# Optimization experiments

Hardware: AMD Instinct MI355X
Metric: run time of the kernel (lower is better)

## Reference

```python
import jax, jax.numpy as jnp
import numpy as np


def setup_inputs() -> dict:
    key = jax.random.key(0)
    ks = jax.random.split(key, 5)
    B, C, D, H, W = 2, 256, 8, 28, 28
    mid = C // 2
    # Kaiming-normal-ish init (std = sqrt(2/fan_in)) for 1x1 conv weights
    def kaiming(k, shape, fan_in):
        return jax.random.normal(k, shape, dtype=jnp.float32) * np.sqrt(2.0 / fan_in)
    x = jax.random.normal(ks[0], (B, C, D, H, W), dtype=jnp.float32)
    w1 = kaiming(ks[1], (mid, C), C)
    w2 = kaiming(ks[2], (mid, C), C)
    w3 = kaiming(ks[3], (mid, C), C)
    w4 = kaiming(ks[4], (C, mid), mid)
    b1 = jnp.zeros((mid,), jnp.float32)
    b2 = jnp.zeros((mid,), jnp.float32)
    b3 = jnp.zeros((mid,), jnp.float32)
    b4 = jnp.zeros((C,), jnp.float32)
    return {"x": x, "w1": w1, "b1": b1, "w2": w2, "b2": b2,
            "w3": w3, "b3": b3, "w4": w4, "b4": b4}


def reference(x, w1, b1, w2, b2, w3, b3, w4, b4):
    # x: [B, C, D, H, W]; 1x1x1 Conv3d == channel matmul over flattened N = D*H*W
    B, C, D, H, W = x.shape
    N = D * H * W
    xf = x.reshape(B, C, N)                                   # [B, C, N]
    # theta: conv1 -> [B, N, mid]
    e1 = jnp.einsum('mc,bcn->bnm', w1, xf) + b1               # [B, N, mid]
    # phi: conv2 -> [B, mid, N]
    e2 = jnp.einsum('mc,bcn->bmn', w2, xf) + b2[:, None]      # [B, mid, N]
    # g: conv3 -> [B, N, mid]
    e3 = jnp.einsum('mc,bcn->bnm', w3, xf) + b3               # [B, N, mid]
    # unscaled attention: softmax over keys (last axis)
    kernel = jnp.einsum('bnm,bmk->bnk', e1, e2)               # [B, N, N]
    kernel = jax.nn.softmax(kernel, axis=2)
    attn = jnp.einsum('bnk,bkm->bnm', kernel, e3)             # [B, N, mid]
    # conv4 (1x1 Conv1d): mid -> C, applied on [B, mid, N]
    y = jnp.einsum('cm,bnm->bcn', w4, attn) + b4[:, None]     # [B, C, N]
    return x + y.reshape(B, C, D, H, W)
```

## Files before the change

### kernel.cpp

```cpp
#include <hip/hip_runtime.h>


#define BB  2
#define CC  256
#define NN  6272
#define MID 128
#define KS  4
#define QB  128
#define NT  (NN / 64)
#define LOG2E 1.4426950408889634f

typedef _Float16 half2_t __attribute__((ext_vector_type(2)));
typedef _Float16 half4_t __attribute__((ext_vector_type(4)));
typedef _Float16 half8_t __attribute__((ext_vector_type(8)));
typedef float    floatx16 __attribute__((ext_vector_type(16)));
typedef int      i32x2 __attribute__((ext_vector_type(2)));
typedef unsigned u32x4 __attribute__((ext_vector_type(4)));

__device__ __forceinline__ void fma4(float4& a, const float4 v, const float s) {
    a.x += v.x * s; a.y += v.y * s; a.z += v.z * s; a.w += v.w * s;
}
__device__ __forceinline__ float dot4(const float4 a, const float4 b) {
    return a.x * b.x + a.y * b.y + a.z * b.z + a.w * b.w;
}
__device__ __forceinline__ unsigned pkrtz(float a, float b) {
    return __builtin_bit_cast(unsigned, __builtin_amdgcn_cvt_pkrtz(a, b));
}

__global__ __launch_bounds__(256, 2) void proj_kernel(
    const float* __restrict__ x,
    const float* __restrict__ w1, const float* __restrict__ bi1,
    const float* __restrict__ w2, const float* __restrict__ bi2,
    const float* __restrict__ w3, const float* __restrict__ bi3,
    _Float16* __restrict__ Qg, _Float16* __restrict__ Kg, _Float16* __restrict__ VtG)
{
    const int t  = threadIdx.x;
    const int n0 = blockIdx.x * 64;
    const int pj = blockIdx.y;
    const int b  = blockIdx.z;
    const float* w  = (pj == 0) ? w1 : (pj == 1) ? w2 : w3;
    const float* bi = (pj == 0) ? bi1 : (pj == 1) ? bi2 : bi3;
    const float qs  = (pj == 0) ? LOG2E : 1.0f;

    __shared__ float xs[CC * 68];
    {
        const float* xb = x + (size_t)b * CC * NN;
        for (int r = t; r < CC * 16; r += 256) {
            int c = r >> 4, j = (r & 15) << 2;
            float4 v = *(const float4*)(xb + (size_t)c * NN + n0 + j);
            *(float4*)&xs[c * 68 + j] = v;
        }
    }
    __syncthreads();

    const int n4 = (t & 15) << 2;
    const int m0 = (t >> 4) << 3;
    float4 acc4[8];
    #pragma unroll
    for (int k = 0; k < 8; ++k) acc4[k] = make_float4(0.f, 0.f, 0.f, 0.f);

    for (int cc = 0; cc < CC; cc += 4) {
        float4 xv[4];
        #pragma unroll
        for (int u = 0; u < 4; ++u)
            xv[u] = *(const float4*)&xs[(cc + u) * 68 + n4];
        #pragma unroll
        for (int k = 0; k < 8; ++k) {
            float4 wq = *(const float4*)(w + (size_t)(m0 + k) * CC + cc);
            fma4(acc4[k], xv[0], wq.x);
            fma4(acc4[k], xv[1], wq.y);
            fma4(acc4[k], xv[2], wq.z);
            fma4(acc4[k], xv[3], wq.w);
        }
    }

    const float* af = (const float*)acc4;
    float bb[8];
    #pragma unroll
    for (int k = 0; k < 8; ++k) bb[k] = bi[m0 + k];

    if (pj < 2) {
        _Float16* eo = ((pj == 0) ? Qg : Kg) + (size_t)b * NN * MID;
        #pragma unroll
        for (int i = 0; i < 4; ++i) {
            half8_t h;
            #pragma unroll
            for (int k = 0; k < 8; ++k) h[k] = (_Float16)((af[k * 4 + i] + bb[k]) * qs);
            *(half8_t*)(eo + (size_t)(n0 + n4 + i) * MID + m0) = h;
        }
    } else {
        _Float16* eo = VtG + (size_t)b * MID * NN;
        #pragma unroll
        for (int k = 0; k < 8; ++k) {
            half4_t h;
            #pragma unroll
            for (int i = 0; i < 4; ++i) h[i] = (_Float16)(af[k * 4 + i] + bb[k]);
            *(half4_t*)(eo + (size_t)(m0 + k) * NN + n0 + n4) = h;
        }
    }
}

__global__ __launch_bounds__(256, 2) void attn_kernel(
    const _Float16* __restrict__ Qg, const _Float16* __restrict__ Kg,
    const _Float16* __restrict__ VtG, _Float16* __restrict__ Opart,
    float* __restrict__ MLg)
{
    const int t    = threadIdx.x;
    const int lane = t & 63;
    const int wave = t >> 6;
    const int l31  = lane & 31;
    const int l5   = lane >> 5;
    const int q0   = blockIdx.x * QB;
    const int sp   = blockIdx.y;
    const int b    = blockIdx.z;
    const int kt0  = (NT * sp) / KS;
    const int kt1  = (NT * (sp + 1)) / KS;

    __shared__ __align__(16) char lds[34816];
    _Float16* Ks  = (_Float16*)lds;
    _Float16* Vt  = (_Float16*)(lds + 17408);
    _Float16* Osh = (_Float16*)lds;

    const _Float16* Qb = Qg + ((size_t)b * NN + q0 + wave * 32) * MID;
    const _Float16* Kb = Kg + (size_t)b * NN * MID;
    const _Float16* Vb = VtG + (size_t)b * MID * NN;

    half8_t qf[8];
    #pragma unroll
    for (int ds = 0; ds < 8; ++ds)
        qf[ds] = *(const half8_t*)(Qb + (size_t)l31 * MID + ds * 16 + l5 * 8);

    floatx16 o[4];
    #pragma unroll
    for (int dt = 0; dt < 4; ++dt)
        #pragma unroll
        for (int j = 0; j < 16; ++j) o[dt][j] = 0.f;
    float m_run = -3.0e38f, l_run = 0.f;

    for (int kt = kt0; kt < kt1; ++kt) {
        const int nk = kt * 64;
        #pragma unroll
        for (int it = 0; it < 4; ++it) {
            int c = it * 256 + t;
            int r = c >> 4, off = (c & 15) * 8;
            *(half8_t*)(Ks + r * 136 + off) =
                *(const half8_t*)(Kb + (size_t)(nk + r) * MID + off);
        }
        #pragma unroll
        for (int it = 0; it < 4; ++it) {
            int c = it * 256 + t;
            int d = c >> 3, off = (c & 7) * 8;
            *(half8_t*)(Vt + d * 68 + off) =
                *(const half8_t*)(Vb + (size_t)d * NN + nk + off);
        }
        __syncthreads();

        floatx16 s0, s1;
        #pragma unroll
        for (int j = 0; j < 16; ++j) { s0[j] = 0.f; s1[j] = 0.f; }
        const _Float16* krow0 = Ks + l31 * 136 + l5 * 8;
        const _Float16* krow1 = Ks + (32 + l31) * 136 + l5 * 8;
        #pragma unroll
        for (int ds = 0; ds < 8; ++ds) {
            s0 = __builtin_amdgcn_mfma_f32_32x32x16_f16(
                     *(const half8_t*)(krow0 + ds * 16), qf[ds], s0, 0, 0, 0);
            s1 = __builtin_amdgcn_mfma_f32_32x32x16_f16(
                     *(const half8_t*)(krow1 + ds * 16), qf[ds], s1, 0, 0, 0);
        }

        float tmax = fmaxf(s0[0], s1[0]);
        #pragma unroll
        for (int j = 1; j < 16; ++j) tmax = fmaxf(tmax, fmaxf(s0[j], s1[j]));
        tmax = fmaxf(tmax, __shfl_xor(tmax, 32));

        if (!__all(tmax <= m_run)) {
            const float m_new = fmaxf(m_run, tmax);
            const float alpha = exp2f(m_run - m_new);
            m_run = m_new;
            l_run *= alpha;
            #pragma unroll
            for (int dt = 0; dt < 4; ++dt)
                #pragma unroll
                for (int j = 0; j < 16; ++j) o[dt][j] *= alpha;
        }

        float psum = 0.f;
        unsigned u0[8], u1[8];
        #pragma unroll
        for (int g = 0; g < 4; ++g) {
            float p0 = exp2f(s0[4 * g + 0] - m_run);
            float p1 = exp2f(s0[4 * g + 1] - m_run);
            float p2 = exp2f(s0[4 * g + 2] - m_run);
            float p3 = exp2f(s0[4 * g + 3] - m_run);
            psum += (p0 + p1) + (p2 + p3);
            u0[g] = pkrtz(p0, p1);
            u1[g] = pkrtz(p2, p3);
        }
        #pragma unroll
        for (int g = 0; g < 4; ++g) {
            float p0 = exp2f(s1[4 * g + 0] - m_run);
            float p1 = exp2f(s1[4 * g + 1] - m_run);
            float p2 = exp2f(s1[4 * g + 2] - m_run);
            float p3 = exp2f(s1[4 * g + 3] - m_run);
            psum += (p0 + p1) + (p2 + p3);
            u0[4 + g] = pkrtz(p0, p1);
            u1[4 + g] = pkrtz(p2, p3);
        }
        psum += __shfl_xor(psum, 32);
        l_run += psum;

        #pragma unroll
        for (int ks = 0; ks < 4; ++ks) {
            i32x2 rA = __builtin_amdgcn_permlane32_swap(
                           (int)u0[2 * ks], (int)u0[2 * ks + 1], false, false);
            i32x2 rB = __builtin_amdgcn_permlane32_swap(
                           (int)u1[2 * ks], (int)u1[2 * ks + 1], false, false);
            u32x4 pw;
            pw[0] = (unsigned)rA[0]; pw[1] = (unsigned)rB[0];
            pw[2] = (unsigned)rA[1]; pw[3] = (unsigned)rB[1];
            half8_t pf = __builtin_bit_cast(half8_t, pw);
            const _Float16* vcol = Vt + ks * 16 + l5 * 8;
            #pragma unroll
            for (int dt = 0; dt < 4; ++dt)
                o[dt] = __builtin_amdgcn_mfma_f32_32x32x16_f16(
                            *(const half8_t*)(vcol + (dt * 32 + l31) * 68), pf,
                            o[dt], 0, 0, 0);
        }
        __syncthreads();
    }

    if (l5 == 0) {
        float* mlb = MLg + ((size_t)(b * KS + sp) * 2) * NN;
        mlb[q0 + wave * 32 + l31]      = m_run;
        mlb[NN + q0 + wave * 32 + l31] = l_run;
    }

    #pragma unroll
    for (int dt = 0; dt < 4; ++dt)
        #pragma unroll
        for (int h = 0; h < 4; ++h) {
            half4_t v;
            #pragma unroll
            for (int i = 0; i < 4; ++i) v[i] = (_Float16)o[dt][4 * h + i];
            *(half4_t*)(Osh + (wave * 32 + l31) * 136 + dt * 32 + 8 * h + 4 * l5) = v;
        }
    __syncthreads();
    _Float16* Ob = Opart + ((size_t)(b * KS + sp) * NN + q0) * MID;
    #pragma unroll
    for (int it = 0; it < 8; ++it) {
        int c = it * 256 + t;
        int q = c >> 4, g = c & 15;
        *(half8_t*)(Ob + (size_t)q * MID + g * 8) =
            *(const half8_t*)(Osh + q * 136 + g * 8);
    }
}

__global__ __launch_bounds__(256, 4) void comb_kernel(
    const _Float16* __restrict__ Opart, const float* __restrict__ MLg,
    _Float16* __restrict__ attnW)
{
    const int t  = threadIdx.x;
    const int b  = blockIdx.y;
    const int q  = blockIdx.x * 32 + (t >> 3);
    const int dg = (t & 7) * 16;

    float mv[KS], lv[KS];
    float m_g = -3.0e38f;
    #pragma unroll
    for (int s = 0; s < KS; ++s) {
        const float* mlb = MLg + ((size_t)(b * KS + s) * 2) * NN;
        mv[s] = mlb[q];
        lv[s] = mlb[NN + q];
        m_g = fmaxf(m_g, mv[s]);
    }
    float lg = 0.f, w[KS];
    #pragma unroll
    for (int s = 0; s < KS; ++s) { w[s] = exp2f(mv[s] - m_g); lg += lv[s] * w[s]; }
    const float inv = 1.0f / lg;

    float acc[16];
    #pragma unroll
    for (int j = 0; j < 16; ++j) acc[j] = 0.f;
    #pragma unroll
    for (int s = 0; s < KS; ++s) {
        const half8_t* Op = (const half8_t*)(Opart + ((size_t)(b * KS + s) * NN + q) * MID + dg);
        half8_t v0 = Op[0], v1 = Op[1];
        #pragma unroll
        for (int j = 0; j < 8; ++j) {
            acc[j]     += (float)v0[j] * w[s];
            acc[8 + j] += (float)v1[j] * w[s];
        }
    }
    half8_t h0, h1;
    #pragma unroll
    for (int j = 0; j < 8; ++j) {
        h0[j] = (_Float16)(acc[j] * inv);
        h1[j] = (_Float16)(acc[8 + j] * inv);
    }
    half8_t* Ow = (half8_t*)(attnW + ((size_t)b * NN + q) * MID + dg);
    Ow[0] = h0; Ow[1] = h1;
}

__global__ __launch_bounds__(256, 2) void epi_kernel(
    const _Float16* __restrict__ attnW, const float* __restrict__ w4,
    const float* __restrict__ b4, const float* __restrict__ x,
    float* __restrict__ out)
{
    const int t  = threadIdx.x;
    const int n0 = blockIdx.x * 64;
    const int b  = blockIdx.y;

    __shared__ float as[64 * 132];
    for (int r = t; r < 64 * 16; r += 256) {
        int q = r >> 4, g = r & 15;
        half8_t v = *(const half8_t*)(attnW + ((size_t)b * NN + n0 + q) * MID + g * 8);
        float* dst = &as[q * 132 + g * 8];
        #pragma unroll
        for (int j = 0; j < 8; ++j) dst[j] = (float)v[j];
    }
    __syncthreads();

    const int n4 = (t & 15) << 2;
    const int c0 = (t >> 4) << 4;
    float4 accE[16];
    #pragma unroll
    for (int k = 0; k < 16; ++k) accE[k] = make_float4(0.f, 0.f, 0.f, 0.f);

    for (int ms = 0; ms < 32; ++ms) {
        float4 av[4];
        #pragma unroll
        for (int i = 0; i < 4; ++i)
            av[i] = *(const float4*)&as[(n4 + i) * 132 + (ms << 2)];
        #pragma unroll
        for (int k = 0; k < 16; ++k) {
            float4 wq = *(const float4*)(w4 + (size_t)(c0 + k) * MID + (ms << 2));
            accE[k].x += dot4(av[0], wq);
            accE[k].y += dot4(av[1], wq);
            accE[k].z += dot4(av[2], wq);
            accE[k].w += dot4(av[3], wq);
        }
    }

    #pragma unroll
    for (int k = 0; k < 16; ++k) {
        const int c = c0 + k;
        const float bv = b4[c];
        const size_t off = ((size_t)b * CC + c) * NN + n0 + n4;
        float4 xr = *(const float4*)(x + off);
        float4 r;
        r.x = accE[k].x + bv + xr.x;
        r.y = accE[k].y + bv + xr.y;
        r.z = accE[k].z + bv + xr.z;
        r.w = accE[k].w + bv + xr.w;
        *(float4*)(out + off) = r;
    }
}

extern "C" void kernel_launch(void* const* d_in, const int* in_sizes, int n_in,
                              void* d_out, int out_size, void* d_ws, size_t ws_size,
                              hipStream_t stream)
{
    const float* x  = (const float*)d_in[0];
    const float* w1 = (const float*)d_in[1];
    const float* b1 = (const float*)d_in[2];
    const float* w2 = (const float*)d_in[3];
    const float* b2 = (const float*)d_in[4];
    const float* w3 = (const float*)d_in[5];
    const float* b3 = (const float*)d_in[6];
    const float* w4 = (const float*)d_in[7];
    const float* b4 = (const float*)d_in[8];
    float* out = (float*)d_out;

    _Float16* Qg    = (_Float16*)d_ws;
    _Float16* Kg    = Qg + (size_t)BB * NN * MID;
    _Float16* VtG   = Kg + (size_t)BB * NN * MID;
    _Float16* attnW = VtG + (size_t)BB * NN * MID;
    float* MLg      = (float*)(attnW + (size_t)BB * NN * MID);
    _Float16* Opart = (_Float16*)d_out;

    proj_kernel<<<dim3(NN / 64, 3, BB), 256, 0, stream>>>(x, w1, b1, w2, b2, w3, b3, Qg, Kg, VtG);
    attn_kernel<<<dim3(NN / QB, KS, BB), 256, 0, stream>>>(Qg, Kg, VtG, Opart, MLg);
    comb_kernel<<<dim3(NN / 32, BB), 256, 0, stream>>>(Opart, MLg, attnW);
    epi_kernel<<<dim3(NN / 64, BB), 256, 0, stream>>>(attnW, w4, b4, x, out);
}
```

Measured before the change: 301.4 us.

## Double-buffer K tiles and prefetch K/V into registers during QK MFMA

Splits the K shared-memory tile into two buffers. Each iteration issues global loads for the current V tile and the next K tile into registers before the QK^T MFMAs, then writes them to LDS after the softmax step. This hides global load latency behind compute. The cost is more LDS (52KB per block), which may cut occupancy below two blocks per CU, plus extra register pressure from the prefetch registers.

```diff
diff --git a/kernel.cpp b/kernel.cpp
--- a/kernel.cpp
+++ b/kernel.cpp
@@ -116,9 +116,10 @@
     const int kt0  = (NT * sp) / KS;
     const int kt1  = (NT * (sp + 1)) / KS;
 
-    __shared__ __align__(16) char lds[34816];
-    _Float16* Ks  = (_Float16*)lds;
-    _Float16* Vt  = (_Float16*)(lds + 17408);
+    __shared__ __align__(16) char lds[52224];
+    _Float16* Ks0 = (_Float16*)lds;
+    _Float16* Ks1 = (_Float16*)(lds + 17408);
+    _Float16* Vt  = (_Float16*)(lds + 34816);
     _Float16* Osh = (_Float16*)lds;
 
     const _Float16* Qb = Qg + ((size_t)b * NN + q0 + wave * 32) * MID;
@@ -137,29 +138,37 @@
         for (int j = 0; j < 16; ++j) o[dt][j] = 0.f;
     float m_run = -3.0e38f, l_run = 0.f;
 
-    for (int kt = kt0; kt < kt1; ++kt) {
+    const int krow_t = t >> 4, koff_t = (t & 15) * 8;
+    const int vd_t   = t >> 3, voff_t = (t & 7) * 8;
+
+    #pragma unroll
+    for (int it = 0; it < 4; ++it) {
+        int r = it * 16 + krow_t;
+        *(half8_t*)(Ks0 + r * 136 + koff_t) =
+            *(const half8_t*)(Kb + (size_t)(kt0 * 64 + r) * MID + koff_t);
+    }
+    __syncthreads();
+
+    for (int kt = kt0, cbuf = 0; kt < kt1; ++kt, cbuf ^= 1) {
         const int nk = kt * 64;
-        #pragma unroll
-        for (int it = 0; it < 4; ++it) {
-            int c = it * 256 + t;
-            int r = c >> 4, off = (c & 15) * 8;
-            *(half8_t*)(Ks + r * 136 + off) =
-                *(const half8_t*)(Kb + (size_t)(nk + r) * MID + off);
-        }
-        #pragma unroll
-        for (int it = 0; it < 4; ++it) {
-            int c = it * 256 + t;
-            int d = c >> 3, off = (c & 7) * 8;
-            *(half8_t*)(Vt + d * 68 + off) =
-                *(const half8_t*)(Vb + (size_t)d * NN + nk + off);
-        }
-        __syncthreads();
+        _Float16* KBcur = cbuf ? Ks1 : Ks0;
+        _Float16* KBnxt = cbuf ? Ks0 : Ks1;
+
+        const int nk2 = (kt + 1 < kt1) ? nk + 64 : nk;
+        half8_t vreg[4], kreg[4];
+        #pragma unroll
+        for (int it = 0; it < 4; ++it)
+            vreg[it] = *(const half8_t*)(Vb + (size_t)(it * 32 + vd_t) * NN + nk + voff_t);
+        #pragma unroll
+        for (int it = 0; it < 4; ++it)
+            kreg[it] = *(const half8_t*)(Kb + (size_t)(nk2 + it * 16 + krow_t) * MID + koff_t);
+        __builtin_amdgcn_sched_barrier(0);
 
         floatx16 s0, s1;
         #pragma unroll
         for (int j = 0; j < 16; ++j) { s0[j] = 0.f; s1[j] = 0.f; }
-        const _Float16* krow0 = Ks + l31 * 136 + l5 * 8;
-        const _Float16* krow1 = Ks + (32 + l31) * 136 + l5 * 8;
+        const _Float16* krow0 = KBcur + l31 * 136 + l5 * 8;
+        const _Float16* krow1 = KBcur + (32 + l31) * 136 + l5 * 8;
         #pragma unroll
         for (int ds = 0; ds < 8; ++ds) {
             s0 = __builtin_amdgcn_mfma_f32_32x32x16_f16(
@@ -208,6 +217,14 @@
         }
         psum += __shfl_xor(psum, 32);
         l_run += psum;
+
+        #pragma unroll
+        for (int it = 0; it < 4; ++it)
+            *(half8_t*)(Vt + (it * 32 + vd_t) * 68 + voff_t) = vreg[it];
+        #pragma unroll
+        for (int it = 0; it < 4; ++it)
+            *(half8_t*)(KBnxt + (it * 16 + krow_t) * 136 + koff_t) = kreg[it];
+        __syncthreads();
 
         #pragma unroll
         for (int ks = 0; ks < 4; ++ks) {
```

After: 302.7 us. About the same (+0.4%).
